# Optimization experiments

Hardware: AMD Instinct MI355X
Metric: run time of the kernel (lower is better)

Reference implementation:

```python
import jax, jax.numpy as jnp
import numpy as np

FLT_BACKWARP = 2.5  # Matching.fltBackwarp for intLevel == 4
NEG_SLOPE = 0.1


def backwarp(ten_input, ten_flow):
    # torch grid_sample(mode='bilinear', padding_mode='zeros', align_corners=True)
    # with grid = base + flow*2/(size-1) is equivalent to sampling at pixel coords
    # (x + u, y + v) with zero padding outside [0, W-1] x [0, H-1].
    B, C, H, W = ten_input.shape
    xs = jnp.arange(W, dtype=ten_input.dtype)
    ys = jnp.arange(H, dtype=ten_input.dtype)
    px = xs[None, None, :] + ten_flow[:, 0]  # [B,H,W]
    py = ys[None, :, None] + ten_flow[:, 1]  # [B,H,W]
    x0 = jnp.floor(px)
    y0 = jnp.floor(py)
    x1 = x0 + 1.0
    y1 = y0 + 1.0
    wx1 = px - x0
    wx0 = 1.0 - wx1
    wy1 = py - y0
    wy0 = 1.0 - wy1

    def gather(ix, iy):
        valid = ((ix >= 0) & (ix <= W - 1) & (iy >= 0) & (iy <= H - 1)).astype(ten_input.dtype)
        ixc = jnp.clip(ix, 0, W - 1).astype(jnp.int32)
        iyc = jnp.clip(iy, 0, H - 1).astype(jnp.int32)
        v = jax.vmap(lambda img, yy, xx: img[:, yy, xx])(ten_input, iyc, ixc)  # [B,C,H,W]
        return v * valid[:, None]

    return (gather(x0, y0) * (wx0 * wy0)[:, None]
            + gather(x1, y0) * (wx1 * wy0)[:, None]
            + gather(x0, y1) * (wx0 * wy1)[:, None]
            + gather(x1, y1) * (wx1 * wy1)[:, None])


def correlation(one, two, stride):
    # FunctionCorrelation: 7x7 displacement window, offsets (-3..3)*stride,
    # zero pad 3*stride, dot over channels / C. Output [B,49,ceil(H/s),ceil(W/s)].
    B, C, H, W = one.shape
    p = 3 * stride
    two_pad = jnp.pad(two, ((0, 0), (0, 0), (p, p), (p, p)))
    one_s = one[:, :, ::stride, ::stride]  # [B,C,Ho,Wo]
    outs = []
    for dj in range(-3, 4):  # channel index k = (dj+3)*7 + (di+3)
        for di in range(-3, 4):
            y0 = p + dj * stride
            x0 = p + di * stride
            shift = two_pad[:, :, y0:y0 + H:stride, x0:x0 + W:stride]
            outs.append(jnp.einsum('bchw,bchw->bhw', one_s, shift))
    return jnp.stack(outs, axis=1) / jnp.asarray(C, one.dtype)


def setup_inputs() -> dict:
    key = jax.random.key(0)
    k1, k2, k3 = jax.random.split(key, 3)
    B, C, H, W = 2, 128, 256, 448
    return {
        'tenOne': jax.random.normal(k1, (B, C, H, W), dtype=jnp.float32),
        'tenTwo': jax.random.normal(k2, (B, C, H, W), dtype=jnp.float32),
        'tenFlow': jax.random.normal(k3, (B, 2, H, W), dtype=jnp.float32),
        'intStride': 1,
    }


def reference(tenOne, tenTwo, tenFlow, intStride):
    warped = backwarp(tenTwo, tenFlow * FLT_BACKWARP)
    corr = correlation(tenOne, warped, int(intStride))
    return jax.nn.leaky_relu(corr, NEG_SLOPE)
```

## Files before the change

### kernel.cpp

```cpp
#include <hip/hip_runtime.h>
#include <hip/hip_bf16.h>

#define BB 2
#define CC 128
#define HH 256
#define WW 448
#define KK 49
#define HWSZ (HH * WW)

#define TWT_BYTES ((size_t)BB * HH * WW * CC * 2)
#define DESC_BYTES ((size_t)BB * HWSZ * 32)

typedef __attribute__((ext_vector_type(8))) short bf16x8;
typedef __attribute__((ext_vector_type(4))) float f32x4;
typedef __attribute__((ext_vector_type(8))) unsigned short u16x8;

static __device__ __forceinline__ short f2bf(float v) {
  __hip_bfloat16 h = __float2bfloat16(v);
  return *reinterpret_cast<short*>(&h);
}
static __device__ __forceinline__ float bf2f(unsigned short u) {
  unsigned int x = ((unsigned int)u) << 16;
  return __uint_as_float(x);
}

__global__ __launch_bounds__(256) void transpose_kernel(
    const float* __restrict__ two, __hip_bfloat16* __restrict__ two_t) {
  __shared__ float lds[128 * 33];
  int bid = blockIdx.x;
  int b = bid / (HWSZ / 32);
  int tile = bid - b * (HWSZ / 32);
  int P0 = tile * 32;

  const float* src = two + (size_t)b * CC * HWSZ + P0;
  int t = threadIdx.x;
  int bc = t >> 3;
  int f = t & 7;
#pragma unroll
  for (int k = 0; k < 4; ++k) {
    int c = bc + k * 32;
    float4 v = *(const float4*)(src + (size_t)c * HWSZ + f * 4);
    float* d = &lds[c * 33 + f * 4];
    d[0] = v.x; d[1] = v.y; d[2] = v.z; d[3] = v.w;
  }
  __syncthreads();

  int q = t & 7;
  int pl = t >> 3;
  int cs = q * 16;
  u16x8 pk0, pk1;
#pragma unroll
  for (int j = 0; j < 8; ++j)
    pk0[j] = (unsigned short)f2bf(lds[(cs + j) * 33 + pl]);
#pragma unroll
  for (int j = 0; j < 8; ++j)
    pk1[j] = (unsigned short)f2bf(lds[(cs + 8 + j) * 33 + pl]);
  char* dst = (char*)two_t + ((size_t)((size_t)b * HWSZ + P0 + pl) * CC + cs) * 2;
  *(u16x8*)dst = pk0;
  *(u16x8*)(dst + 16) = pk1;
}

__global__ __launch_bounds__(256) void flowprep(
    const float* __restrict__ flow, float* __restrict__ desc) {
  int idx = blockIdx.x * 256 + threadIdx.x;
  int x = idx % WW;
  int y = (idx / WW) % HH;
  int b = idx / HWSZ;

  float fx = flow[(size_t)(b * 2 + 0) * HWSZ + y * WW + x] * 2.5f;
  float fy = flow[(size_t)(b * 2 + 1) * HWSZ + y * WW + x] * 2.5f;
  float px = (float)x + fx;
  float py = (float)y + fy;
  float x0f = floorf(px), y0f = floorf(py);
  int x0 = (int)x0f, y0 = (int)y0f;
  int x1 = x0 + 1, y1 = y0 + 1;
  float wx1 = px - x0f, wx0 = 1.0f - wx1;
  float wy1 = py - y0f, wy0 = 1.0f - wy1;
  bool vx0 = (x0 >= 0) && (x0 < WW);
  bool vx1 = (x1 >= 0) && (x1 < WW);
  bool vy0 = (y0 >= 0) && (y0 < HH);
  bool vy1 = (y1 >= 0) && (y1 < HH);
  float w00 = (vx0 && vy0) ? wx0 * wy0 : 0.0f;
  float w01 = (vx1 && vy0) ? wx1 * wy0 : 0.0f;
  float w10 = (vx0 && vy1) ? wx0 * wy1 : 0.0f;
  float w11 = (vx1 && vy1) ? wx1 * wy1 : 0.0f;
  int cx0 = min(max(x0, 0), WW - 1);
  int cx1 = min(max(x1, 0), WW - 1);
  int cy0 = min(max(y0, 0), HH - 1);
  int cy1 = min(max(y1, 0), HH - 1);

  float* d = desc + (size_t)idx * 8;
  *(float4*)d = make_float4(w00, w01, w10, w11);
  int4 o = make_int4(cy0 * WW + cx0, cy0 * WW + cx1, cy1 * WW + cx0,
                     cy1 * WW + cx1);
  *(int4*)(d + 4) = o;
}

#define YTB 8
#define NROWS 14
#define NPOS 22
#define ROWCH (NPOS * 16)
#define CHUNKS (NROWS * ROWCH)

__global__ __launch_bounds__(512, 2) void corr_fused(
    const float* __restrict__ one, const __hip_bfloat16* __restrict__ two_t,
    const float* __restrict__ desc, float* __restrict__ out) {
  __shared__ uint4 ldsb[CHUNKS];

  int bid = blockIdx.x;
  int wg = (bid & 7) * 224 + (bid >> 3);
  int b = wg / 896;
  int rem = wg - b * 896;
  int xt = rem >> 5;
  int yt = rem & 31;
  int ybase = yt * YTB;
  int X0 = xt * 16;
  int tid = threadIdx.x;
  int w = tid >> 6;
  int l = tid & 63;
  int lp = l & 15;
  int lg = l >> 4;
  int y = ybase + w;

  const char* tb = (const char*)two_t + (size_t)b * HWSZ * (CC * 2);
  const float* dbase = desc + (size_t)b * HWSZ * 8;

#pragma unroll
  for (int k = 0; k < 10; ++k) {
    int ci = tid + k * 512;
    if (ci < CHUNKS) {
      int row = ci / ROWCH;
      int r2 = ci - row * ROWCH;
      int p = r2 >> 4;
      int cw = r2 & 15;
      int yy = ybase - 3 + row;
      int x = X0 + p - 3;
      bool vpix = (yy >= 0) && (yy < HH) && (x >= 0) && (x < WW);
      int yyc = min(max(yy, 0), HH - 1);
      int xc = min(max(x, 0), WW - 1);
      const float* dp = dbase + (size_t)(yyc * WW + xc) * 8;
      float4 wv = *(const float4*)dp;
      int4 ov = *(const int4*)(dp + 4);

      u16x8 ca = *(const u16x8*)(tb + (size_t)ov.x * 256 + cw * 16);
      u16x8 cb = *(const u16x8*)(tb + (size_t)ov.y * 256 + cw * 16);
      u16x8 cc = *(const u16x8*)(tb + (size_t)ov.z * 256 + cw * 16);
      u16x8 cd = *(const u16x8*)(tb + (size_t)ov.w * 256 + cw * 16);

      u16x8 pk;
#pragma unroll
      for (int e = 0; e < 8; ++e) {
        float v = wv.x * bf2f((unsigned short)ca[e]) +
                  wv.y * bf2f((unsigned short)cb[e]) +
                  wv.z * bf2f((unsigned short)cc[e]) +
                  wv.w * bf2f((unsigned short)cd[e]);
        pk[e] = (unsigned short)f2bf(v);
      }
      if (!vpix) pk = (u16x8){0, 0, 0, 0, 0, 0, 0, 0};
      *(u16x8*)((char*)ldsb + ((ci * 16) ^ ((p & 15) << 4))) = pk;
    }
  }

  const float* Abase = one + ((size_t)(b * CC) * HH + y) * WW + X0 + lp;
  bf16x8 afr[4];
#pragma unroll
  for (int t = 0; t < 4; ++t)
#pragma unroll
    for (int j = 0; j < 8; ++j)
      afr[t][j] = f2bf(Abase[(size_t)(t * 32 + lg * 8 + j) * HWSZ]);

  __syncthreads();

  int p1 = (lp + 16 < 21) ? (lp + 16) : 21;
  int cosw0[4], cosw1[4];
#pragma unroll
  for (int t = 0; t < 4; ++t) {
    int co = t * 64 + lg * 16;
    cosw0[t] = co ^ ((lp & 15) << 4);
    cosw1[t] = co ^ ((p1 & 15) << 4);
  }

  f32x4 acc[7][2] = {};
#pragma unroll
  for (int dj = 0; dj < 7; ++dj) {
    int rl = w + dj;
    int b0 = (rl * NPOS + lp) << 8;
    int b1 = (rl * NPOS + p1) << 8;
#pragma unroll
    for (int t = 0; t < 4; ++t) {
      bf16x8 v0 = *(const bf16x8*)((const char*)ldsb + (b0 + cosw0[t]));
      bf16x8 v1 = *(const bf16x8*)((const char*)ldsb + (b1 + cosw1[t]));
      acc[dj][0] = __builtin_amdgcn_mfma_f32_16x16x32_bf16(afr[t], v0,
                                                           acc[dj][0], 0, 0, 0);
      acc[dj][1] = __builtin_amdgcn_mfma_f32_16x16x32_bf16(afr[t], v1,
                                                           acc[dj][1], 0, 0, 0);
    }
  }

  __syncthreads();
  float* sc = (float*)ldsb;
#pragma unroll
  for (int dj = 0; dj < 7; ++dj) {
#pragma unroll
    for (int nt = 0; nt < 2; ++nt) {
      int post = lp + 16 * nt;
#pragma unroll
      for (int r = 0; r < 4; ++r) {
        int xlc = 4 * lg + r;
        int di = post - xlc;
        if (di >= 0 && di <= 6) {
          int k = dj * 7 + di;
          sc[k * 128 + w * 16 + ((xlc + k) & 15)] = acc[dj][nt][r];
        }
      }
    }
  }
  __syncthreads();

  float* ob = out + (size_t)(b * KK) * HWSZ + (size_t)ybase * WW + X0;
#pragma unroll
  for (int i = 0; i < 13; ++i) {
    int e = tid + i * 512;
    if (e < KK * 128) {
      int k = e >> 7;
      int yr = (e >> 4) & 7;
      int px = e & 15;
      float v = sc[k * 128 + yr * 16 + ((px + k) & 15)] * (1.0f / 128.0f);
      v = (v > 0.0f) ? v : 0.1f * v;
      ob[(size_t)k * HWSZ + yr * WW + px] = v;
    }
  }
}

extern "C" void kernel_launch(void* const* d_in, const int* in_sizes, int n_in,
                              void* d_out, int out_size, void* d_ws,
                              size_t ws_size, hipStream_t stream) {
  const float* tenOne = (const float*)d_in[0];
  const float* tenTwo = (const float*)d_in[1];
  const float* tenFlow = (const float*)d_in[2];

  __hip_bfloat16* two_t = (__hip_bfloat16*)d_ws;
  float* desc = (float*)((char*)d_ws + TWT_BYTES);

  transpose_kernel<<<BB * (HWSZ / 32), 256, 0, stream>>>(tenTwo, two_t);
  flowprep<<<BB * HWSZ / 256, 256, 0, stream>>>(tenFlow, desc);
  corr_fused<<<1792, 512, 0, stream>>>(tenOne, two_t, desc, (float*)d_out);
}
```

Baseline: 117.6 us.

## Software-pipeline descriptor loads ahead of gather chunks and raise occupancy bound

Splits the staging loop into separate descriptor-load and gather/blend phases. Descriptor loads for later chunks are issued ahead of processing earlier ones, and sched_barrier fences keep the compiler from reordering the phases. This hides the dependent-load latency chain (desc -> offsets -> gathers). Launch bounds also rise from 2 to 4 waves-per-EU minimum, which restricts register use. Holding more descriptors live at once increases register pressure and may cause spills under the tighter bound.

```diff
diff --git a/kernel.cpp b/kernel.cpp
--- a/kernel.cpp
+++ b/kernel.cpp
@@ -102,7 +102,7 @@
 #define ROWCH (NPOS * 16)
 #define CHUNKS (NROWS * ROWCH)
 
-__global__ __launch_bounds__(512, 2) void corr_fused(
+__global__ __launch_bounds__(512, 4) void corr_fused(
     const float* __restrict__ one, const __hip_bfloat16* __restrict__ two_t,
     const float* __restrict__ desc, float* __restrict__ out) {
   __shared__ uint4 ldsb[CHUNKS];
@@ -125,41 +125,73 @@
   const char* tb = (const char*)two_t + (size_t)b * HWSZ * (CC * 2);
   const float* dbase = desc + (size_t)b * HWSZ * 8;
 
-#pragma unroll
-  for (int k = 0; k < 10; ++k) {
-    int ci = tid + k * 512;
-    if (ci < CHUNKS) {
-      int row = ci / ROWCH;
-      int r2 = ci - row * ROWCH;
-      int p = r2 >> 4;
-      int cw = r2 & 15;
-      int yy = ybase - 3 + row;
-      int x = X0 + p - 3;
-      bool vpix = (yy >= 0) && (yy < HH) && (x >= 0) && (x < WW);
-      int yyc = min(max(yy, 0), HH - 1);
-      int xc = min(max(x, 0), WW - 1);
-      const float* dp = dbase + (size_t)(yyc * WW + xc) * 8;
-      float4 wv = *(const float4*)dp;
-      int4 ov = *(const int4*)(dp + 4);
-
-      u16x8 ca = *(const u16x8*)(tb + (size_t)ov.x * 256 + cw * 16);
-      u16x8 cb = *(const u16x8*)(tb + (size_t)ov.y * 256 + cw * 16);
-      u16x8 cc = *(const u16x8*)(tb + (size_t)ov.z * 256 + cw * 16);
-      u16x8 cd = *(const u16x8*)(tb + (size_t)ov.w * 256 + cw * 16);
-
-      u16x8 pk;
-#pragma unroll
-      for (int e = 0; e < 8; ++e) {
-        float v = wv.x * bf2f((unsigned short)ca[e]) +
-                  wv.y * bf2f((unsigned short)cb[e]) +
-                  wv.z * bf2f((unsigned short)cc[e]) +
-                  wv.w * bf2f((unsigned short)cd[e]);
-        pk[e] = (unsigned short)f2bf(v);
-      }
-      if (!vpix) pk = (u16x8){0, 0, 0, 0, 0, 0, 0, 0};
-      *(u16x8*)((char*)ldsb + ((ci * 16) ^ ((p & 15) << 4))) = pk;
-    }
-  }
+#define DESC_LOAD(K, WV, OV)                                  \
+  {                                                           \
+    int ci = tid + (K)*512;                                   \
+    if (ci < CHUNKS) {                                        \
+      int row = ci / ROWCH;                                   \
+      int r2 = ci - row * ROWCH;                              \
+      int p_ = r2 >> 4;                                       \
+      int yy = ybase - 3 + row;                               \
+      int x_ = X0 + p_ - 3;                                   \
+      int yyc = min(max(yy, 0), HH - 1);                      \
+      int xc = min(max(x_, 0), WW - 1);                       \
+      const float* dp = dbase + (size_t)(yyc * WW + xc) * 8;  \
+      WV = *(const float4*)dp;                                \
+      OV = *(const int4*)(dp + 4);                            \
+    }                                                         \
+  }
+
+#define CHUNK_PROC(K, WV, OV)                                              \
+  {                                                                        \
+    int ci = tid + (K)*512;                                                \
+    if (ci < CHUNKS) {                                                     \
+      int row = ci / ROWCH;                                                \
+      int r2 = ci - row * ROWCH;                                           \
+      int p_ = r2 >> 4;                                                    \
+      int cw = r2 & 15;                                                    \
+      int yy = ybase - 3 + row;                                            \
+      int x_ = X0 + p_ - 3;                                                \
+      bool vpix = (yy >= 0) && (yy < HH) && (x_ >= 0) && (x_ < WW);        \
+      u16x8 ca = *(const u16x8*)(tb + (size_t)(OV).x * 256 + cw * 16);     \
+      u16x8 cb = *(const u16x8*)(tb + (size_t)(OV).y * 256 + cw * 16);     \
+      u16x8 cc = *(const u16x8*)(tb + (size_t)(OV).z * 256 + cw * 16);     \
+      u16x8 cd = *(const u16x8*)(tb + (size_t)(OV).w * 256 + cw * 16);     \
+      u16x8 pk;                                                            \
+      _Pragma("unroll") for (int e = 0; e < 8; ++e) {                      \
+        float v = (WV).x * bf2f((unsigned short)ca[e]) +                   \
+                  (WV).y * bf2f((unsigned short)cb[e]) +                   \
+                  (WV).z * bf2f((unsigned short)cc[e]) +                   \
+                  (WV).w * bf2f((unsigned short)cd[e]);                    \
+        pk[e] = (unsigned short)f2bf(v);                                   \
+      }                                                                    \
+      if (!vpix) pk = (u16x8){0, 0, 0, 0, 0, 0, 0, 0};                     \
+      *(u16x8*)((char*)ldsb + ((ci * 16) ^ ((p_ & 15) << 4))) = pk;        \
+    }                                                                      \
+  }
+
+  float4 wA0 = {}, wA1 = {}, wA2 = {}, wA3 = {};
+  int4 oA0 = {}, oA1 = {}, oA2 = {}, oA3 = {};
+  float4 wB0 = {}, wB1 = {}, wB2 = {}, wB3 = {};
+  int4 oB0 = {}, oB1 = {}, oB2 = {}, oB3 = {};
+  float4 wC0 = {}, wC1 = {};
+  int4 oC0 = {}, oC1 = {};
+
+  DESC_LOAD(0, wA0, oA0) DESC_LOAD(1, wA1, oA1)
+  DESC_LOAD(2, wA2, oA2) DESC_LOAD(3, wA3, oA3)
+  __builtin_amdgcn_sched_barrier(0);
+  DESC_LOAD(4, wB0, oB0) DESC_LOAD(5, wB1, oB1)
+  DESC_LOAD(6, wB2, oB2) DESC_LOAD(7, wB3, oB3)
+  __builtin_amdgcn_sched_barrier(0);
+  CHUNK_PROC(0, wA0, oA0) CHUNK_PROC(1, wA1, oA1)
+  CHUNK_PROC(2, wA2, oA2) CHUNK_PROC(3, wA3, oA3)
+  __builtin_amdgcn_sched_barrier(0);
+  DESC_LOAD(8, wC0, oC0) DESC_LOAD(9, wC1, oC1)
+  __builtin_amdgcn_sched_barrier(0);
+  CHUNK_PROC(4, wB0, oB0) CHUNK_PROC(5, wB1, oB1)
+  CHUNK_PROC(6, wB2, oB2) CHUNK_PROC(7, wB3, oB3)
+  __builtin_amdgcn_sched_barrier(0);
+  CHUNK_PROC(8, wC0, oC0) CHUNK_PROC(9, wC1, oC1)
 
   const float* Abase = one + ((size_t)(b * CC) * HH + y) * WW + X0 + lp;
   bf16x8 afr[4];
@@ -230,6 +262,8 @@
       ob[(size_t)k * HWSZ + yr * WW + px] = v;
     }
   }
+#undef DESC_LOAD
+#undef CHUNK_PROC
 }
 
 extern "C" void kernel_launch(void* const* d_in, const int* in_sizes, int n_in,
```

Measured after the change: 118.9 us. Within noise of the previous version (+1.2%).
